# Performance work log

Measured on AMD Instinct MI355X. Metric: run time of the kernel, lower is better.

The kernel has to match this reference:

```python
import jax, jax.numpy as jnp
import numpy as np

B, S, E, H = 2, 2048, 512, 8
DH = E // H
SCALE = DH ** -0.5
TEMPERATURE = 1.0
LN_EPS = 1e-5


def setup_inputs() -> dict:
    key = jax.random.key(0)
    ks = jax.random.split(key, 12)
    s = E ** -0.5
    return {
        "q": jax.random.normal(ks[0], (B, S, E), jnp.float32),
        "k": jax.random.normal(ks[1], (B, S, E), jnp.float32),
        "v": jax.random.normal(ks[2], (B, S, E), jnp.float32),
        "Wq": jax.random.normal(ks[3], (E, E), jnp.float32) * s,
        "bq": jnp.zeros((E,), jnp.float32),
        "Wk": jax.random.normal(ks[4], (E, E), jnp.float32) * s,
        "bk": jnp.zeros((E,), jnp.float32),
        "Wv": jax.random.normal(ks[5], (E, E), jnp.float32) * s,
        "bv": jnp.zeros((E,), jnp.float32),
        "Wo": jax.random.normal(ks[6], (E, E), jnp.float32) * s,
        "bo": jnp.zeros((E,), jnp.float32),
        "ln_g": jnp.ones((E,), jnp.float32),
        "ln_b": jnp.zeros((E,), jnp.float32),
    }


def reference(q, k, v, Wq, bq, Wk, bk, Wv, bv, Wo, bo, ln_g, ln_b):
    # QKV projections (nn.Linear: x @ W.T + b)
    qh = (q @ Wq.T + bq).reshape(B, S, H, DH).transpose(0, 2, 1, 3)  # [B,H,S,Dh]
    kh = (k @ Wk.T + bk).reshape(B, S, H, DH).transpose(0, 2, 1, 3)
    vh = (v @ Wv.T + bv).reshape(B, S, H, DH).transpose(0, 2, 1, 3)
    # attention scores [B,H,S,S], scaled then divided by temperature
    scores = jnp.einsum('bhqd,bhkd->bhqk', qh, kh) * (SCALE / TEMPERATURE)
    attn = jax.nn.softmax(scores, axis=-1)
    # dropout is identity in eval mode
    x = jnp.einsum('bhqk,bhkd->bhqd', attn, vh)  # [B,H,S,Dh]
    x = x.transpose(0, 2, 1, 3).reshape(B, S, E)
    # out projection + LayerNorm
    y = x @ Wo.T + bo
    mu = jnp.mean(y, axis=-1, keepdims=True)
    var = jnp.var(y, axis=-1, keepdims=True)
    out = (y - mu) * jax.lax.rsqrt(var + LN_EPS) * ln_g + ln_b
    return out
```

## Files before the change

### kernel.cpp

```cpp
#include <hip/hip_runtime.h>
#include <hip/hip_bf16.h>
#include <stdint.h>

#define B_ 2
#define S_ 2048
#define E_ 512
#define H_ 8
#define DH_ 64
#define BH_ (B_*H_)
#define M_ (B_*S_)

typedef short short8 __attribute__((ext_vector_type(8)));
typedef float f32x4 __attribute__((ext_vector_type(4)));
typedef float f32x16 __attribute__((ext_vector_type(16)));
typedef int int4v __attribute__((ext_vector_type(4)));

#define QSCALE 0.18033688011112042f

#if __has_builtin(__builtin_amdgcn_exp2f)
#define EXP2(x) __builtin_amdgcn_exp2f(x)
#else
#define EXP2(x) exp2f(x)
#endif

__device__ __forceinline__ float asf(uint32_t u) { return __builtin_bit_cast(float, u); }
__device__ __forceinline__ uint32_t asu(float f) { return __builtin_bit_cast(uint32_t, f); }

__device__ __forceinline__ ushort f2bf(float f) {
  uint32_t u = __builtin_bit_cast(uint32_t, f);
  u += 0x7fffu + ((u >> 16) & 1u);
  return (ushort)(u >> 16);
}

__device__ __forceinline__ uint32_t cvtpk(float lo, float hi) {
  uint32_t r;
  asm("v_cvt_pk_bf16_f32 %0, %1, %2" : "=v"(r) : "v"(lo), "v"(hi));
  return r;
}

__device__ __forceinline__ void swap32(uint32_t a, uint32_t b, uint32_t& o0, uint32_t& o1) {
#if __has_builtin(__builtin_amdgcn_permlane32_swap)
  typedef int v2i __attribute__((ext_vector_type(2)));
  v2i r = __builtin_amdgcn_permlane32_swap((int)a, (int)b, false, false);
  o0 = (uint32_t)r.x; o1 = (uint32_t)r.y;
#else
  int laneid = (int)(threadIdx.x & 63);
  uint32_t pa = (uint32_t)__shfl_xor((int)a, 32, 64);
  uint32_t pb = (uint32_t)__shfl_xor((int)b, 32, 64);
  bool hi = laneid >= 32;
  o0 = hi ? pb : a;
  o1 = hi ? b : pa;
#endif
}

__device__ __forceinline__ void gll16(const void* g, void* l) {
  __builtin_amdgcn_global_load_lds((const __attribute__((address_space(1))) void*)g,
                                   (__attribute__((address_space(3))) void*)l,
                                   16, 0, 0);
}

struct CvtArgs {
  const float* s[7];
  ushort* d[7];
  int nq[7];
};

__global__ __launch_bounds__(256) void cvt_kernel(CvtArgs a) {
  int seg = blockIdx.y;
  int i = blockIdx.x * 256 + threadIdx.x;
  if (i >= a.nq[seg]) return;
  float4 v = ((const float4*)a.s[seg])[i];
  ushort4 o;
  o.x = f2bf(v.x); o.y = f2bf(v.y); o.z = f2bf(v.z); o.w = f2bf(v.w);
  ((ushort4*)a.d[seg])[i] = o;
}

template<int EPI>
__global__ __launch_bounds__(256) void gemm_bt(
    const ushort* __restrict__ A0, const ushort* __restrict__ A1, const ushort* __restrict__ A2,
    const ushort* __restrict__ W0, const ushort* __restrict__ W1, const ushort* __restrict__ W2,
    const float* __restrict__ bias0, const float* __restrict__ bias1, const float* __restrict__ bias2,
    ushort* O0, ushort* O1, ushort* O2, float* Yout)
{
  const int K = E_;
  int z = blockIdx.z;
  const ushort* A = (z == 0) ? A0 : ((z == 1) ? A1 : A2);
  const ushort* W = (z == 0) ? W0 : ((z == 1) ? W1 : W2);
  const float* bias = (z == 0) ? bias0 : ((z == 1) ? bias1 : bias2);
  ushort* O = (z == 0) ? O0 : ((z == 1) ? O1 : O2);
  float scale = (EPI == 0 && z == 0) ? QSCALE : 1.0f;

  int n0 = blockIdx.x * 128, m0 = blockIdx.y * 128;
  int tid = threadIdx.x, lane = tid & 63, wid = tid >> 6;
  int wm = wid >> 1, wn = wid & 1;

  __shared__ ushort As[128 * 32];
  __shared__ ushort Bs[128 * 32];

  f32x4 acc[4][4];
#pragma unroll
  for (int i = 0; i < 4; ++i)
#pragma unroll
    for (int j = 0; j < 4; ++j)
      acc[i][j] = (f32x4){0.f, 0.f, 0.f, 0.f};

  for (int kt = 0; kt < K / 32; ++kt) {
    int k0 = kt * 32;
#pragma unroll
    for (int c = 0; c < 2; ++c) {
      int f = c * 256 + tid;
      int r = f >> 2;
      int lc = (f & 3) ^ ((r >> 1) & 3);
      gll16(A + (m0 + r) * K + k0 + lc * 8, (char*)As + (c * 256 + wid * 64) * 16);
    }
#pragma unroll
    for (int c = 0; c < 2; ++c) {
      int f = c * 256 + tid;
      int r = f >> 2;
      int lc = (f & 3) ^ ((r >> 1) & 3);
      gll16(W + (n0 + r) * K + k0 + lc * 8, (char*)Bs + (c * 256 + wid * 64) * 16);
    }
    __syncthreads();

    short8 af[4], bf[4];
#pragma unroll
    for (int fm = 0; fm < 4; ++fm) {
      int r = wm * 64 + fm * 16 + (lane & 15);
      int phys = (lane >> 4) ^ ((r >> 1) & 3);
      af[fm] = *(const short8*)((const char*)As + r * 64 + phys * 16);
    }
#pragma unroll
    for (int fn = 0; fn < 4; ++fn) {
      int r = wn * 64 + fn * 16 + (lane & 15);
      int phys = (lane >> 4) ^ ((r >> 1) & 3);
      bf[fn] = *(const short8*)((const char*)Bs + r * 64 + phys * 16);
    }
#pragma unroll
    for (int fm = 0; fm < 4; ++fm)
#pragma unroll
      for (int fn = 0; fn < 4; ++fn)
        acc[fm][fn] = __builtin_amdgcn_mfma_f32_16x16x32_bf16(af[fm], bf[fn], acc[fm][fn], 0, 0, 0);
    __syncthreads();
  }

#pragma unroll
  for (int fm = 0; fm < 4; ++fm) {
#pragma unroll
    for (int fn = 0; fn < 4; ++fn) {
#pragma unroll
      for (int j = 0; j < 4; ++j) {
        int m = m0 + wm * 64 + fm * 16 + (lane >> 4) * 4 + j;
        int n = n0 + wn * 64 + fn * 16 + (lane & 15);
        float v = (acc[fm][fn][j] + bias[n]) * scale;
        if constexpr (EPI == 0) {
          int b = m >> 11, s = m & (S_ - 1);
          int h = n >> 6, d = n & 63;
          O[((b * H_ + h) * S_ + s) * DH_ + d] = f2bf(v);
        } else {
          Yout[m * E_ + n] = v;
        }
      }
    }
  }
}

__global__ __launch_bounds__(256) void vtrans(const ushort* __restrict__ Vh, ushort* __restrict__ Vt) {
  int bh = blockIdx.y;
  int s0 = blockIdx.x * 64;
  __shared__ ushort t[64][72];
  int tid = threadIdx.x;
  const ushort* src = Vh + ((size_t)bh * S_ + s0) * DH_;
  int r = tid >> 2, c0 = (tid & 3) * 16;
#pragma unroll
  for (int i = 0; i < 2; ++i) {
    short8 v = *(const short8*)(src + r * DH_ + c0 + i * 8);
#pragma unroll
    for (int kx = 0; kx < 8; ++kx) t[r][c0 + i * 8 + kx] = (ushort)v[kx];
  }
  __syncthreads();
  int d = tid >> 2, j0 = (tid & 3) * 16;
  ushort* dst = Vt + ((size_t)bh * DH_ + d) * S_ + s0 + j0;
#pragma unroll
  for (int i = 0; i < 2; ++i) {
    short8 o;
#pragma unroll
    for (int kx = 0; kx < 8; ++kx) o[kx] = (short)t[j0 + i * 8 + kx][d];
    *(short8*)(dst + i * 8) = o;
  }
}

__global__ __launch_bounds__(256, 4) void attn_kernel(const ushort* __restrict__ Qh,
                                                      const ushort* __restrict__ Kh,
                                                      const ushort* __restrict__ Vt,
                                                      ushort* __restrict__ X) {
  int bh = blockIdx.x;
  int q0 = blockIdx.y * 64;
  int tid = threadIdx.x, lane = tid & 63, wid = tid >> 6;
  int wq = wid & 1, wk = wid >> 1;
  int hi = lane >> 5;

  __shared__ ushort lds_[16384];
  char* L = (char*)lds_;

  const ushort* Kg = Kh + (size_t)bh * S_ * DH_;
  const ushort* Vg = Vt + (size_t)bh * DH_ * S_;

  int q = q0 + wq * 32 + (lane & 31);
  const ushort* Qrow = Qh + ((size_t)bh * S_ + q) * DH_;
  short8 qf[4];
#pragma unroll
  for (int ds = 0; ds < 4; ++ds)
    qf[ds] = *(const short8*)(Qrow + ds * 16 + hi * 8);

  f32x16 sacc, oacc[2];
#pragma unroll
  for (int r = 0; r < 16; ++r) { oacc[0][r] = 0.f; oacc[1][r] = 0.f; }
  float m_r = -INFINITY, l_r = 0.f;

  const int NT = 32;

#define STAGE(buf, t)                                                          \
  do {                                                                         \
    _Pragma("unroll")                                                          \
    for (int w2 = 0; w2 < 2; ++w2) {                                           \
      int kb = w2 * 1024 + (t) * 32;                                           \
      char* Kd = L + (buf) * 16384 + w2 * 8192;                                \
      char* Vd = Kd + 4096;                                                    \
      {                                                                        \
        int r = tid >> 3, lc = (tid & 7) ^ (r & 7);                            \
        gll16(Kg + (size_t)(kb + r) * DH_ + lc * 8, Kd + wid * 1024);          \
      }                                                                        \
      {                                                                        \
        int rho = tid >> 3, l2 = (tid & 7) ^ (rho & 7);                        \
        int d = rho + ((l2 >> 2) << 5), kc = (l2 & 3) * 8;                     \
        gll16(Vg + (size_t)d * S_ + kb + kc, Vd + wid * 1024);                 \
      }                                                                        \
    }                                                                          \
  } while (0)

  STAGE(0, 0);
  __syncthreads();

  for (int t = 0; t < NT; ++t) {
    int cur = t & 1;
    if (t + 1 < NT) STAGE(cur ^ 1, t + 1);

    const char* Kt = L + cur * 16384 + wk * 8192;
    const char* Vtile = Kt + 4096;

#pragma unroll
    for (int r = 0; r < 16; ++r) sacc[r] = 0.f;
    int kl = lane & 31;
#pragma unroll
    for (int ds = 0; ds < 4; ++ds) {
      short8 kf = *(const short8*)(Kt + kl * 128 + (((2 * ds + hi) ^ (kl & 7)) * 16));
      sacc = __builtin_amdgcn_mfma_f32_32x32x16_bf16(kf, qf[ds], sacc, 0, 0, 0);
    }

    float mx = fmaxf(fmaxf(sacc[0], sacc[1]), sacc[2]);
    mx = fmaxf(mx, fmaxf(fmaxf(sacc[3], sacc[4]), sacc[5]));
    mx = fmaxf(mx, fmaxf(fmaxf(sacc[6], sacc[7]), sacc[8]));
    mx = fmaxf(mx, fmaxf(fmaxf(sacc[9], sacc[10]), sacc[11]));
    mx = fmaxf(mx, fmaxf(fmaxf(sacc[12], sacc[13]), sacc[14]));
    mx = fmaxf(mx, sacc[15]);
    bool skip = __all(mx - m_r <= 8.0f);
    if (!skip) {
      uint32_t e0, e1;
      swap32(asu(mx), asu(mx), e0, e1);
      float mnew = fmaxf(m_r, fmaxf(asf(e0), asf(e1)));
      float scf = EXP2(m_r - mnew);
      m_r = mnew;
      l_r *= scf;
#pragma unroll
      for (int dblk = 0; dblk < 2; ++dblk)
#pragma unroll
        for (int r = 0; r < 16; ++r) oacc[dblk][r] *= scf;
    }
    float rs0 = 0.f, rs1 = 0.f;
#pragma unroll
    for (int r = 0; r < 16; r += 2) {
      float p0 = EXP2(sacc[r] - m_r);
      float p1 = EXP2(sacc[r + 1] - m_r);
      sacc[r] = p0; sacc[r + 1] = p1;
      rs0 += p0; rs1 += p1;
    }
    float rs = rs0 + rs1;
    {
      uint32_t e0, e1;
      swap32(asu(rs), asu(rs), e0, e1);
      l_r += asf(e0) + asf(e1);
    }

    uint32_t w[8];
#pragma unroll
    for (int i = 0; i < 8; ++i)
      w[i] = cvtpk(sacc[2 * i], sacc[2 * i + 1]);

    short8 pf[2];
#pragma unroll
    for (int ks = 0; ks < 2; ++ks) {
      uint32_t e01, e45, e23, e67;
      swap32(w[4 * ks + 0], w[4 * ks + 2], e01, e45);
      swap32(w[4 * ks + 1], w[4 * ks + 3], e23, e67);
      int4v iv;
      iv[0] = (int)e01; iv[1] = (int)e23; iv[2] = (int)e45; iv[3] = (int)e67;
      pf[ks] = __builtin_bit_cast(short8, iv);
    }

#pragma unroll
    for (int ks = 0; ks < 2; ++ks) {
      int rho = lane & 31;
#pragma unroll
      for (int dblk = 0; dblk < 2; ++dblk) {
        int lch = dblk * 4 + 2 * ks + hi;
        short8 vf = *(const short8*)(Vtile + rho * 128 + ((lch ^ (rho & 7)) * 16));
        oacc[dblk] = __builtin_amdgcn_mfma_f32_32x32x16_bf16(vf, pf[ks], oacc[dblk], 0, 0, 0);
      }
    }

    __syncthreads();
  }
#undef STAGE

  float* fl = (float*)L;
  if (wk == 1) {
#pragma unroll
    for (int dblk = 0; dblk < 2; ++dblk)
#pragma unroll
      for (int r = 0; r < 16; ++r)
        fl[((wq * 2 + dblk) * 16 + r) * 64 + lane] = oacc[dblk][r];
    fl[4096 + wq * 64 + lane] = m_r;
    fl[4224 + wq * 64 + lane] = l_r;
  }
  __syncthreads();
  if (wk == 0) {
    float m1 = fl[4096 + wq * 64 + lane];
    float l1 = fl[4224 + wq * 64 + lane];
    float mstar = fmaxf(m_r, m1);
    float a0 = EXP2(m_r - mstar);
    float a1 = EXP2(m1 - mstar);
    float lstar = l_r * a0 + l1 * a1;
    float invl = 1.0f / lstar;
    int b = bh >> 3, h = bh & 7;
    int s = q0 + wq * 32 + (lane & 31);
    ushort* Xrow = X + (size_t)(b * S_ + s) * E_ + h * DH_;
#pragma unroll
    for (int dblk = 0; dblk < 2; ++dblk) {
#pragma unroll
      for (int i = 0; i < 8; ++i) {
        int r0 = 2 * i, r1 = 2 * i + 1;
        float o0 = (oacc[dblk][r0] * a0 + fl[((wq * 2 + dblk) * 16 + r0) * 64 + lane] * a1) * invl;
        float o1 = (oacc[dblk][r1] * a0 + fl[((wq * 2 + dblk) * 16 + r1) * 64 + lane] * a1) * invl;
        int d = dblk * 32 + (r0 & 3) + 8 * (r0 >> 2) + 4 * hi;
        *(uint32_t*)(Xrow + d) = cvtpk(o0, o1);
      }
    }
  }
}

__global__ __launch_bounds__(256) void ln_kernel(const float* __restrict__ Y,
                                                 const float* __restrict__ g,
                                                 const float* __restrict__ bta,
                                                 float* __restrict__ out) {
  int tid = threadIdx.x, lane = tid & 63, wid = tid >> 6;
  int row = blockIdx.x * 4 + wid;
  const float* y = Y + (size_t)row * E_;
  float4 v0 = *(const float4*)(y + lane * 8);
  float4 v1 = *(const float4*)(y + lane * 8 + 4);
  float s = v0.x + v0.y + v0.z + v0.w + v1.x + v1.y + v1.z + v1.w;
  float q = v0.x * v0.x + v0.y * v0.y + v0.z * v0.z + v0.w * v0.w +
            v1.x * v1.x + v1.y * v1.y + v1.z * v1.z + v1.w * v1.w;
#pragma unroll
  for (int msk = 1; msk < 64; msk <<= 1) {
    s += __shfl_xor(s, msk);
    q += __shfl_xor(q, msk);
  }
  float mu = s * (1.f / E_);
  float var = q * (1.f / E_) - mu * mu;
  float inv = rsqrtf(var + 1e-5f);
  float4 g0 = *(const float4*)(g + lane * 8);
  float4 g1 = *(const float4*)(g + lane * 8 + 4);
  float4 b0 = *(const float4*)(bta + lane * 8);
  float4 b1 = *(const float4*)(bta + lane * 8 + 4);
  float4 o0, o1;
  o0.x = (v0.x - mu) * inv * g0.x + b0.x;
  o0.y = (v0.y - mu) * inv * g0.y + b0.y;
  o0.z = (v0.z - mu) * inv * g0.z + b0.z;
  o0.w = (v0.w - mu) * inv * g0.w + b0.w;
  o1.x = (v1.x - mu) * inv * g1.x + b1.x;
  o1.y = (v1.y - mu) * inv * g1.y + b1.y;
  o1.z = (v1.z - mu) * inv * g1.z + b1.z;
  o1.w = (v1.w - mu) * inv * g1.w + b1.w;
  float* op = out + (size_t)row * E_;
  *(float4*)(op + lane * 8) = o0;
  *(float4*)(op + lane * 8 + 4) = o1;
}

extern "C" void kernel_launch(void* const* d_in, const int* in_sizes, int n_in,
                              void* d_out, int out_size, void* d_ws, size_t ws_size,
                              hipStream_t stream) {
  const float* q = (const float*)d_in[0];
  const float* k = (const float*)d_in[1];
  const float* v = (const float*)d_in[2];
  const float* Wq = (const float*)d_in[3];
  const float* bq = (const float*)d_in[4];
  const float* Wk = (const float*)d_in[5];
  const float* bk = (const float*)d_in[6];
  const float* Wv = (const float*)d_in[7];
  const float* bv = (const float*)d_in[8];
  const float* Wo = (const float*)d_in[9];
  const float* bo = (const float*)d_in[10];
  const float* ln_g = (const float*)d_in[11];
  const float* ln_b = (const float*)d_in[12];

  char* ws = (char*)d_ws;
  const size_t MB = 1024 * 1024;
  ushort* qb  = (ushort*)(ws + 0 * MB);
  ushort* kb  = (ushort*)(ws + 4 * MB);
  ushort* vb  = (ushort*)(ws + 8 * MB);
  ushort* Wqb = (ushort*)(ws + 12 * MB);
  ushort* Wkb = (ushort*)(ws + 12 * MB + 512 * 1024);
  ushort* Wvb = (ushort*)(ws + 13 * MB);
  ushort* Wob = (ushort*)(ws + 13 * MB + 512 * 1024);
  ushort* Qhb = (ushort*)(ws + 14 * MB);
  ushort* Khb = (ushort*)(ws + 18 * MB);
  ushort* Vhb = (ushort*)(ws + 22 * MB);
  ushort* Vtb = (ushort*)(ws + 26 * MB);
  ushort* Xb  = (ushort*)(ws + 30 * MB);
  float*  Yb  = (float*)(ws + 34 * MB);

  CvtArgs ca;
  ca.s[0] = q;  ca.d[0] = qb;  ca.nq[0] = (B_ * S_ * E_) / 4;
  ca.s[1] = k;  ca.d[1] = kb;  ca.nq[1] = (B_ * S_ * E_) / 4;
  ca.s[2] = v;  ca.d[2] = vb;  ca.nq[2] = (B_ * S_ * E_) / 4;
  ca.s[3] = Wq; ca.d[3] = Wqb; ca.nq[3] = (E_ * E_) / 4;
  ca.s[4] = Wk; ca.d[4] = Wkb; ca.nq[4] = (E_ * E_) / 4;
  ca.s[5] = Wv; ca.d[5] = Wvb; ca.nq[5] = (E_ * E_) / 4;
  ca.s[6] = Wo; ca.d[6] = Wob; ca.nq[6] = (E_ * E_) / 4;

  cvt_kernel<<<dim3(2048, 7), dim3(256), 0, stream>>>(ca);

  gemm_bt<0><<<dim3(4, 32, 3), dim3(256), 0, stream>>>(
      qb, kb, vb, Wqb, Wkb, Wvb, bq, bk, bv, Qhb, Khb, Vhb, (float*)nullptr);

  vtrans<<<dim3(S_ / 64, BH_), dim3(256), 0, stream>>>(Vhb, Vtb);

  attn_kernel<<<dim3(BH_, S_ / 64), dim3(256), 0, stream>>>(Qhb, Khb, Vtb, Xb);

  gemm_bt<1><<<dim3(4, 32, 1), dim3(256), 0, stream>>>(
      Xb, Xb, Xb, Wob, Wob, Wob, bo, bo, bo,
      (ushort*)nullptr, (ushort*)nullptr, (ushort*)nullptr, Yb);

  ln_kernel<<<dim3(M_ / 4), dim3(256), 0, stream>>>(Yb, ln_g, ln_b, (float*)d_out);
}
```

Baseline: 77.65 us.

## Fuse V transpose into QKV GEMM epilogue and triple-buffer attention K/V loads

The QKV projection GEMM now writes V directly in transposed [BH, DH, S] layout, which removes the separate vtrans kernel launch and its extra global round trip. The attention kernel moves from a double-buffered LDS pipeline to a three-stage one that prefetches two tiles ahead. It uses explicit vmcnt waits with a raw s_barrier instead of a trailing __syncthreads, and raises wave priority around the MFMA blocks. LDS per block grows to 48KB and launch bounds drop to 3 blocks per SIMD, so occupancy may fall. The transposed-V stores in the GEMM epilogue are strided along s, which may coalesce poorly.

```diff
diff --git a/kernel.cpp b/kernel.cpp
--- a/kernel.cpp
+++ b/kernel.cpp
@@ -155,7 +155,10 @@
         if constexpr (EPI == 0) {
           int b = m >> 11, s = m & (S_ - 1);
           int h = n >> 6, d = n & 63;
-          O[((b * H_ + h) * S_ + s) * DH_ + d] = f2bf(v);
+          if (z == 2)
+            O[((b * H_ + h) * DH_ + d) * S_ + s] = f2bf(v);
+          else
+            O[((b * H_ + h) * S_ + s) * DH_ + d] = f2bf(v);
         } else {
           Yout[m * E_ + n] = v;
         }
@@ -164,32 +167,7 @@
   }
 }
 
-__global__ __launch_bounds__(256) void vtrans(const ushort* __restrict__ Vh, ushort* __restrict__ Vt) {
-  int bh = blockIdx.y;
-  int s0 = blockIdx.x * 64;
-  __shared__ ushort t[64][72];
-  int tid = threadIdx.x;
-  const ushort* src = Vh + ((size_t)bh * S_ + s0) * DH_;
-  int r = tid >> 2, c0 = (tid & 3) * 16;
-#pragma unroll
-  for (int i = 0; i < 2; ++i) {
-    short8 v = *(const short8*)(src + r * DH_ + c0 + i * 8);
-#pragma unroll
-    for (int kx = 0; kx < 8; ++kx) t[r][c0 + i * 8 + kx] = (ushort)v[kx];
-  }
-  __syncthreads();
-  int d = tid >> 2, j0 = (tid & 3) * 16;
-  ushort* dst = Vt + ((size_t)bh * DH_ + d) * S_ + s0 + j0;
-#pragma unroll
-  for (int i = 0; i < 2; ++i) {
-    short8 o;
-#pragma unroll
-    for (int kx = 0; kx < 8; ++kx) o[kx] = (short)t[j0 + i * 8 + kx][d];
-    *(short8*)(dst + i * 8) = o;
-  }
-}
-
-__global__ __launch_bounds__(256, 4) void attn_kernel(const ushort* __restrict__ Qh,
+__global__ __launch_bounds__(256, 3) void attn_kernel(const ushort* __restrict__ Qh,
                                                       const ushort* __restrict__ Kh,
                                                       const ushort* __restrict__ Vt,
                                                       ushort* __restrict__ X) {
@@ -199,7 +177,7 @@
   int wq = wid & 1, wk = wid >> 1;
   int hi = lane >> 5;
 
-  __shared__ ushort lds_[16384];
+  __shared__ ushort lds_[24576];
   char* L = (char*)lds_;
 
   const ushort* Kg = Kh + (size_t)bh * S_ * DH_;
@@ -238,24 +216,36 @@
     }                                                                          \
   } while (0)
 
+  asm volatile("s_waitcnt vmcnt(0)" ::: "memory");
   STAGE(0, 0);
-  __syncthreads();
-
+  STAGE(1, 1);
+
+  int rb = 0;
   for (int t = 0; t < NT; ++t) {
-    int cur = t & 1;
-    if (t + 1 < NT) STAGE(cur ^ 1, t + 1);
-
-    const char* Kt = L + cur * 16384 + wk * 8192;
+    if (t < NT - 1) asm volatile("s_waitcnt vmcnt(4)" ::: "memory");
+    else            asm volatile("s_waitcnt vmcnt(0)" ::: "memory");
+    __builtin_amdgcn_s_barrier();
+    asm volatile("" ::: "memory");
+    __builtin_amdgcn_sched_barrier(0);
+
+    if (t + 2 < NT) {
+      int sb = rb + 2; if (sb >= 3) sb -= 3;
+      STAGE(sb, t + 2);
+    }
+
+    const char* Kt = L + rb * 16384 + wk * 8192;
     const char* Vtile = Kt + 4096;
 
 #pragma unroll
     for (int r = 0; r < 16; ++r) sacc[r] = 0.f;
     int kl = lane & 31;
+    __builtin_amdgcn_s_setprio(1);
 #pragma unroll
     for (int ds = 0; ds < 4; ++ds) {
       short8 kf = *(const short8*)(Kt + kl * 128 + (((2 * ds + hi) ^ (kl & 7)) * 16));
       sacc = __builtin_amdgcn_mfma_f32_32x32x16_bf16(kf, qf[ds], sacc, 0, 0, 0);
     }
+    __builtin_amdgcn_s_setprio(0);
 
     float mx = fmaxf(fmaxf(sacc[0], sacc[1]), sacc[2]);
     mx = fmaxf(mx, fmaxf(fmaxf(sacc[3], sacc[4]), sacc[5]));
@@ -307,6 +297,7 @@
       pf[ks] = __builtin_bit_cast(short8, iv);
     }
 
+    __builtin_amdgcn_s_setprio(1);
 #pragma unroll
     for (int ks = 0; ks < 2; ++ks) {
       int rho = lane & 31;
@@ -317,10 +308,13 @@
         oacc[dblk] = __builtin_amdgcn_mfma_f32_32x32x16_bf16(vf, pf[ks], oacc[dblk], 0, 0, 0);
       }
     }
-
-    __syncthreads();
+    __builtin_amdgcn_s_setprio(0);
+
+    rb = (rb + 1 == 3) ? 0 : rb + 1;
   }
 #undef STAGE
+
+  __syncthreads();
 
   float* fl = (float*)L;
   if (wk == 1) {
@@ -424,7 +418,6 @@
   ushort* Wob = (ushort*)(ws + 13 * MB + 512 * 1024);
   ushort* Qhb = (ushort*)(ws + 14 * MB);
   ushort* Khb = (ushort*)(ws + 18 * MB);
-  ushort* Vhb = (ushort*)(ws + 22 * MB);
   ushort* Vtb = (ushort*)(ws + 26 * MB);
   ushort* Xb  = (ushort*)(ws + 30 * MB);
   float*  Yb  = (float*)(ws + 34 * MB);
@@ -441,9 +434,7 @@
   cvt_kernel<<<dim3(2048, 7), dim3(256), 0, stream>>>(ca);
 
   gemm_bt<0><<<dim3(4, 32, 3), dim3(256), 0, stream>>>(
-      qb, kb, vb, Wqb, Wkb, Wvb, bq, bk, bv, Qhb, Khb, Vhb, (float*)nullptr);
-
-  vtrans<<<dim3(S_ / 64, BH_), dim3(256), 0, stream>>>(Vhb, Vtb);
+      qb, kb, vb, Wqb, Wkb, Wvb, bq, bk, bv, Qhb, Khb, Vtb, (float*)nullptr);
 
   attn_kernel<<<dim3(BH_, S_ / 64), dim3(256), 0, stream>>>(Qhb, Khb, Vtb, Xb);
 
```

After: 81.49 us. 4.9% more time.

## Split attention KV range across four wave groups with 512-thread blocks

Applied to the files above, without the earlier changes.

The attention kernel moves to 512 threads (8 waves), splitting the key range four ways instead of two. Each wave group now runs 16 tiles instead of 32, with per-wave staging of either K or V and a doubled LDS buffer. The four partial softmax states are merged at the end through LDS. s_setprio is wrapped around the MFMA sections. The aim is a shorter serial loop per block and more waves to hide latency, at the cost of more LDS per block, lower block occupancy and a larger merge step.

```diff
diff --git a/kernel.cpp b/kernel.cpp
--- a/kernel.cpp
+++ b/kernel.cpp
@@ -189,7 +189,7 @@
   }
 }
 
-__global__ __launch_bounds__(256, 4) void attn_kernel(const ushort* __restrict__ Qh,
+__global__ __launch_bounds__(512, 4) void attn_kernel(const ushort* __restrict__ Qh,
                                                       const ushort* __restrict__ Kh,
                                                       const ushort* __restrict__ Vt,
                                                       ushort* __restrict__ X) {
@@ -199,7 +199,7 @@
   int wq = wid & 1, wk = wid >> 1;
   int hi = lane >> 5;
 
-  __shared__ ushort lds_[16384];
+  __shared__ ushort lds_[32768];
   char* L = (char*)lds_;
 
   const ushort* Kg = Kh + (size_t)bh * S_ * DH_;
@@ -217,23 +217,26 @@
   for (int r = 0; r < 16; ++r) { oacc[0][r] = 0.f; oacc[1][r] = 0.f; }
   float m_r = -INFINITY, l_r = 0.f;
 
-  const int NT = 32;
+  const int NT = 16;
 
 #define STAGE(buf, t)                                                          \
   do {                                                                         \
-    _Pragma("unroll")                                                          \
-    for (int w2 = 0; w2 < 2; ++w2) {                                           \
-      int kb = w2 * 1024 + (t) * 32;                                           \
-      char* Kd = L + (buf) * 16384 + w2 * 8192;                                \
-      char* Vd = Kd + 4096;                                                    \
-      {                                                                        \
-        int r = tid >> 3, lc = (tid & 7) ^ (r & 7);                            \
-        gll16(Kg + (size_t)(kb + r) * DH_ + lc * 8, Kd + wid * 1024);          \
+    int kb = wk * 512 + (t) * 32;                                              \
+    char* tb = L + (buf) * 32768 + wk * 8192;                                  \
+    if (wq == 0) {                                                             \
+      _Pragma("unroll")                                                        \
+      for (int kk = 0; kk < 4; ++kk) {                                         \
+        int r = kk * 8 + (lane >> 3), c = lane & 7;                            \
+        int lc = c ^ (r & 7);                                                  \
+        gll16(Kg + (size_t)(kb + r) * DH_ + lc * 8, tb + kk * 1024);           \
       }                                                                        \
-      {                                                                        \
-        int rho = tid >> 3, l2 = (tid & 7) ^ (rho & 7);                        \
+    } else {                                                                   \
+      _Pragma("unroll")                                                        \
+      for (int kk = 0; kk < 4; ++kk) {                                         \
+        int rho = kk * 8 + (lane >> 3), c = lane & 7;                          \
+        int l2 = c ^ (rho & 7);                                                \
         int d = rho + ((l2 >> 2) << 5), kc = (l2 & 3) * 8;                     \
-        gll16(Vg + (size_t)d * S_ + kb + kc, Vd + wid * 1024);                 \
+        gll16(Vg + (size_t)d * S_ + kb + kc, tb + 4096 + kk * 1024);           \
       }                                                                        \
     }                                                                          \
   } while (0)
@@ -245,17 +248,19 @@
     int cur = t & 1;
     if (t + 1 < NT) STAGE(cur ^ 1, t + 1);
 
-    const char* Kt = L + cur * 16384 + wk * 8192;
+    const char* Kt = L + cur * 32768 + wk * 8192;
     const char* Vtile = Kt + 4096;
 
 #pragma unroll
     for (int r = 0; r < 16; ++r) sacc[r] = 0.f;
     int kl = lane & 31;
+    __builtin_amdgcn_s_setprio(1);
 #pragma unroll
     for (int ds = 0; ds < 4; ++ds) {
       short8 kf = *(const short8*)(Kt + kl * 128 + (((2 * ds + hi) ^ (kl & 7)) * 16));
       sacc = __builtin_amdgcn_mfma_f32_32x32x16_bf16(kf, qf[ds], sacc, 0, 0, 0);
     }
+    __builtin_amdgcn_s_setprio(0);
 
     float mx = fmaxf(fmaxf(sacc[0], sacc[1]), sacc[2]);
     mx = fmaxf(mx, fmaxf(fmaxf(sacc[3], sacc[4]), sacc[5]));
@@ -307,6 +312,7 @@
       pf[ks] = __builtin_bit_cast(short8, iv);
     }
 
+    __builtin_amdgcn_s_setprio(1);
 #pragma unroll
     for (int ks = 0; ks < 2; ++ks) {
       int rho = lane & 31;
@@ -317,29 +323,50 @@
         oacc[dblk] = __builtin_amdgcn_mfma_f32_32x32x16_bf16(vf, pf[ks], oacc[dblk], 0, 0, 0);
       }
     }
+    __builtin_amdgcn_s_setprio(0);
 
     __syncthreads();
   }
 #undef STAGE
 
   float* fl = (float*)L;
-  if (wk == 1) {
+  if (wk != 0) {
+    int pb = ((wk - 1) * 2 + wq) * 2;
 #pragma unroll
     for (int dblk = 0; dblk < 2; ++dblk)
 #pragma unroll
       for (int r = 0; r < 16; ++r)
-        fl[((wq * 2 + dblk) * 16 + r) * 64 + lane] = oacc[dblk][r];
-    fl[4096 + wq * 64 + lane] = m_r;
-    fl[4224 + wq * 64 + lane] = l_r;
+        fl[(pb + dblk) * 1024 + r * 64 + lane] = oacc[dblk][r];
+    fl[12288 + ((wk - 1) * 2 + wq) * 64 + lane] = m_r;
+    fl[12672 + ((wk - 1) * 2 + wq) * 64 + lane] = l_r;
   }
   __syncthreads();
   if (wk == 0) {
-    float m1 = fl[4096 + wq * 64 + lane];
-    float l1 = fl[4224 + wq * 64 + lane];
-    float mstar = fmaxf(m_r, m1);
+    float mm[3], ll[3];
+#pragma unroll
+    for (int i = 0; i < 3; ++i) {
+      mm[i] = fl[12288 + (i * 2 + wq) * 64 + lane];
+      ll[i] = fl[12672 + (i * 2 + wq) * 64 + lane];
+    }
+    float mstar = fmaxf(fmaxf(m_r, mm[0]), fmaxf(mm[1], mm[2]));
     float a0 = EXP2(m_r - mstar);
-    float a1 = EXP2(m1 - mstar);
-    float lstar = l_r * a0 + l1 * a1;
+    float lstar = l_r * a0;
+    float aa[3];
+#pragma unroll
+    for (int i = 0; i < 3; ++i) {
+      aa[i] = EXP2(mm[i] - mstar);
+      lstar += ll[i] * aa[i];
+    }
+#pragma unroll
+    for (int dblk = 0; dblk < 2; ++dblk)
+#pragma unroll
+      for (int r = 0; r < 16; ++r) {
+        float o = oacc[dblk][r] * a0;
+#pragma unroll
+        for (int i = 0; i < 3; ++i)
+          o += fl[((i * 2 + wq) * 2 + dblk) * 1024 + r * 64 + lane] * aa[i];
+        oacc[dblk][r] = o;
+      }
     float invl = 1.0f / lstar;
     int b = bh >> 3, h = bh & 7;
     int s = q0 + wq * 32 + (lane & 31);
@@ -349,8 +376,8 @@
 #pragma unroll
       for (int i = 0; i < 8; ++i) {
         int r0 = 2 * i, r1 = 2 * i + 1;
-        float o0 = (oacc[dblk][r0] * a0 + fl[((wq * 2 + dblk) * 16 + r0) * 64 + lane] * a1) * invl;
-        float o1 = (oacc[dblk][r1] * a0 + fl[((wq * 2 + dblk) * 16 + r1) * 64 + lane] * a1) * invl;
+        float o0 = oacc[dblk][r0] * invl;
+        float o1 = oacc[dblk][r1] * invl;
         int d = dblk * 32 + (r0 & 3) + 8 * (r0 >> 2) + 4 * hi;
         *(uint32_t*)(Xrow + d) = cvtpk(o0, o1);
       }
@@ -445,7 +472,7 @@
 
   vtrans<<<dim3(S_ / 64, BH_), dim3(256), 0, stream>>>(Vhb, Vtb);
 
-  attn_kernel<<<dim3(BH_, S_ / 64), dim3(256), 0, stream>>>(Qhb, Khb, Vtb, Xb);
+  attn_kernel<<<dim3(BH_, S_ / 64), dim3(512), 0, stream>>>(Qhb, Khb, Vtb, Xb);
 
   gemm_bt<1><<<dim3(4, 32, 1), dim3(256), 0, stream>>>(
       Xb, Xb, Xb, Wob, Wob, Wob, bo, bo, bo,
```

New measurement: 78.39 us. About the same (+0.9%).

## Make attention waves self-stage private K/V tiles without block barriers

Applied to the files above, without the earlier changes.

Each attention block now has two waves covering 32 queries instead of four waves covering 64. Each wave splits the key range and loads its own K/V tiles into a private LDS double buffer. In-loop __syncthreads are replaced by per-wave s_waitcnt vmcnt counts, and s_setprio is raised around the MFMA sections. This removes block-wide barriers from the main loop, at the cost of each wave issuing more global loads and Q/K/V reuse being shared across fewer queries per block.

```diff
diff --git a/kernel.cpp b/kernel.cpp
--- a/kernel.cpp
+++ b/kernel.cpp
@@ -189,28 +189,26 @@
   }
 }
 
-__global__ __launch_bounds__(256, 4) void attn_kernel(const ushort* __restrict__ Qh,
+__global__ __launch_bounds__(128, 2) void attn_kernel(const ushort* __restrict__ Qh,
                                                       const ushort* __restrict__ Kh,
                                                       const ushort* __restrict__ Vt,
                                                       ushort* __restrict__ X) {
   int bh = blockIdx.x;
-  int q0 = blockIdx.y * 64;
-  int tid = threadIdx.x, lane = tid & 63, wid = tid >> 6;
-  int wq = wid & 1, wk = wid >> 1;
-  int hi = lane >> 5;
+  int q0 = blockIdx.y * 32;
+  int tid = threadIdx.x, lane = tid & 63, wk = tid >> 6;
+  int hi = lane >> 5, kl = lane & 31;
 
   __shared__ ushort lds_[16384];
-  char* L = (char*)lds_;
+  char* L = (char*)lds_ + wk * 16384;
 
   const ushort* Kg = Kh + (size_t)bh * S_ * DH_;
   const ushort* Vg = Vt + (size_t)bh * DH_ * S_;
 
-  int q = q0 + wq * 32 + (lane & 31);
-  const ushort* Qrow = Qh + ((size_t)bh * S_ + q) * DH_;
+  const ushort* Qrow = Qh + ((size_t)bh * S_ + q0 + kl) * DH_ + hi * 8;
   short8 qf[4];
 #pragma unroll
   for (int ds = 0; ds < 4; ++ds)
-    qf[ds] = *(const short8*)(Qrow + ds * 16 + hi * 8);
+    qf[ds] = *(const short8*)(Qrow + ds * 16);
 
   f32x16 sacc, oacc[2];
 #pragma unroll
@@ -221,41 +219,47 @@
 
 #define STAGE(buf, t)                                                          \
   do {                                                                         \
+    int kb = wk * 1024 + (t) * 32;                                             \
+    char* Kd = L + (buf) * 8192;                                               \
+    char* Vd = Kd + 4096;                                                      \
     _Pragma("unroll")                                                          \
-    for (int w2 = 0; w2 < 2; ++w2) {                                           \
-      int kb = w2 * 1024 + (t) * 32;                                           \
-      char* Kd = L + (buf) * 16384 + w2 * 8192;                                \
-      char* Vd = Kd + 4096;                                                    \
-      {                                                                        \
-        int r = tid >> 3, lc = (tid & 7) ^ (r & 7);                            \
-        gll16(Kg + (size_t)(kb + r) * DH_ + lc * 8, Kd + wid * 1024);          \
-      }                                                                        \
-      {                                                                        \
-        int rho = tid >> 3, l2 = (tid & 7) ^ (rho & 7);                        \
-        int d = rho + ((l2 >> 2) << 5), kc = (l2 & 3) * 8;                     \
-        gll16(Vg + (size_t)d * S_ + kb + kc, Vd + wid * 1024);                 \
-      }                                                                        \
+    for (int i = 0; i < 4; ++i) {                                              \
+      int r = i * 8 + (lane >> 3), c = (lane & 7) ^ (r & 7);                   \
+      gll16(Kg + (size_t)(kb + r) * DH_ + c * 8, Kd + i * 1024);               \
+    }                                                                          \
+    _Pragma("unroll")                                                          \
+    for (int i = 0; i < 4; ++i) {                                              \
+      int rho = i * 8 + (lane >> 3), l2 = (lane & 7) ^ (rho & 7);              \
+      int d = rho + ((l2 >> 2) << 5), kc = (l2 & 3) * 8;                       \
+      gll16(Vg + (size_t)d * S_ + kb + kc, Vd + i * 1024);                     \
     }                                                                          \
   } while (0)
 
+  asm volatile("s_waitcnt vmcnt(0)" ::: "memory");
   STAGE(0, 0);
-  __syncthreads();
 
   for (int t = 0; t < NT; ++t) {
     int cur = t & 1;
-    if (t + 1 < NT) STAGE(cur ^ 1, t + 1);
-
-    const char* Kt = L + cur * 16384 + wk * 8192;
+    if (t + 1 < NT) {
+      STAGE(cur ^ 1, t + 1);
+      asm volatile("s_waitcnt vmcnt(8)" ::: "memory");
+    } else {
+      asm volatile("s_waitcnt vmcnt(0)" ::: "memory");
+    }
+    __builtin_amdgcn_sched_barrier(0);
+
+    const char* Kt = L + cur * 8192;
     const char* Vtile = Kt + 4096;
 
 #pragma unroll
     for (int r = 0; r < 16; ++r) sacc[r] = 0.f;
-    int kl = lane & 31;
+    __builtin_amdgcn_s_setprio(1);
 #pragma unroll
     for (int ds = 0; ds < 4; ++ds) {
       short8 kf = *(const short8*)(Kt + kl * 128 + (((2 * ds + hi) ^ (kl & 7)) * 16));
       sacc = __builtin_amdgcn_mfma_f32_32x32x16_bf16(kf, qf[ds], sacc, 0, 0, 0);
     }
+    __builtin_amdgcn_s_setprio(0);
 
     float mx = fmaxf(fmaxf(sacc[0], sacc[1]), sacc[2]);
     mx = fmaxf(mx, fmaxf(fmaxf(sacc[3], sacc[4]), sacc[5]));
@@ -307,6 +311,7 @@
       pf[ks] = __builtin_bit_cast(short8, iv);
     }
 
+    __builtin_amdgcn_s_setprio(1);
 #pragma unroll
     for (int ks = 0; ks < 2; ++ks) {
       int rho = lane & 31;
@@ -317,40 +322,40 @@
         oacc[dblk] = __builtin_amdgcn_mfma_f32_32x32x16_bf16(vf, pf[ks], oacc[dblk], 0, 0, 0);
       }
     }
-
-    __syncthreads();
+    __builtin_amdgcn_s_setprio(0);
   }
 #undef STAGE
 
-  float* fl = (float*)L;
+  float* fl = (float*)lds_;
+  __syncthreads();
   if (wk == 1) {
 #pragma unroll
     for (int dblk = 0; dblk < 2; ++dblk)
 #pragma unroll
       for (int r = 0; r < 16; ++r)
-        fl[((wq * 2 + dblk) * 16 + r) * 64 + lane] = oacc[dblk][r];
-    fl[4096 + wq * 64 + lane] = m_r;
-    fl[4224 + wq * 64 + lane] = l_r;
+        fl[(dblk * 16 + r) * 64 + lane] = oacc[dblk][r];
+    fl[2048 + lane] = m_r;
+    fl[2112 + lane] = l_r;
   }
   __syncthreads();
   if (wk == 0) {
-    float m1 = fl[4096 + wq * 64 + lane];
-    float l1 = fl[4224 + wq * 64 + lane];
+    float m1 = fl[2048 + lane];
+    float l1 = fl[2112 + lane];
     float mstar = fmaxf(m_r, m1);
     float a0 = EXP2(m_r - mstar);
     float a1 = EXP2(m1 - mstar);
     float lstar = l_r * a0 + l1 * a1;
     float invl = 1.0f / lstar;
     int b = bh >> 3, h = bh & 7;
-    int s = q0 + wq * 32 + (lane & 31);
+    int s = q0 + kl;
     ushort* Xrow = X + (size_t)(b * S_ + s) * E_ + h * DH_;
 #pragma unroll
     for (int dblk = 0; dblk < 2; ++dblk) {
 #pragma unroll
       for (int i = 0; i < 8; ++i) {
         int r0 = 2 * i, r1 = 2 * i + 1;
-        float o0 = (oacc[dblk][r0] * a0 + fl[((wq * 2 + dblk) * 16 + r0) * 64 + lane] * a1) * invl;
-        float o1 = (oacc[dblk][r1] * a0 + fl[((wq * 2 + dblk) * 16 + r1) * 64 + lane] * a1) * invl;
+        float o0 = (oacc[dblk][r0] * a0 + fl[(dblk * 16 + r0) * 64 + lane] * a1) * invl;
+        float o1 = (oacc[dblk][r1] * a0 + fl[(dblk * 16 + r1) * 64 + lane] * a1) * invl;
         int d = dblk * 32 + (r0 & 3) + 8 * (r0 >> 2) + 4 * hi;
         *(uint32_t*)(Xrow + d) = cvtpk(o0, o1);
       }
@@ -445,7 +450,7 @@
 
   vtrans<<<dim3(S_ / 64, BH_), dim3(256), 0, stream>>>(Vhb, Vtb);
 
-  attn_kernel<<<dim3(BH_, S_ / 64), dim3(256), 0, stream>>>(Qhb, Khb, Vtb, Xb);
+  attn_kernel<<<dim3(BH_, S_ / 32), dim3(128), 0, stream>>>(Qhb, Khb, Vtb, Xb);
 
   gemm_bt<1><<<dim3(4, 32, 1), dim3(256), 0, stream>>>(
       Xb, Xb, Xb, Wob, Wob, Wob, bo, bo, bo,
```

Result: slower. 80.83 us (+4.1%).
